# Kernel optimization log

Measured on AMD Instinct MI355X. Metric: run time of the kernel, lower is better.

Reference implementation:

```python
import jax, jax.numpy as jnp
import numpy as np

B, S, H = 2, 2048, 1024
NH = 16
HD = H // NH
MLP = 32


def setup_inputs() -> dict:
    key = jax.random.key(0)
    ks = jax.random.split(key, 24)
    def lin(k, fan_in, shape):
        bound = 1.0 / np.sqrt(fan_in)
        return jax.random.uniform(k, shape, jnp.float32, -bound, bound)
    return {
        "hidden_states": jax.random.normal(ks[0], (B, S, H), jnp.float32),
        "importance_scores": jax.random.uniform(ks[1], (B, S), jnp.float32),
        "wq": lin(ks[2], H, (H, H)), "bq": lin(ks[3], H, (H,)),
        "wk": lin(ks[4], H, (H, H)), "bk": lin(ks[5], H, (H,)),
        "wv": lin(ks[6], H, (H, H)), "bv": lin(ks[7], H, (H,)),
        "wo": lin(ks[8], H, (H, H)), "bo": lin(ks[9], H, (H,)),
        "rw1": lin(ks[10], 1, (1, MLP)), "rb1": lin(ks[11], 1, (MLP,)),
        "rw2": lin(ks[12], MLP, (MLP, NH)), "rb2": lin(ks[13], MLP, (NH,)),
        "aw1": lin(ks[14], 1, (1, MLP)), "ab1": lin(ks[15], 1, (MLP,)),
        "aw2": lin(ks[16], MLP, (MLP, NH)), "ab2": lin(ks[17], MLP, (NH,)),
        "log_temperature": jnp.zeros((NH,), jnp.float32),
        "ln_g": jnp.ones((H,), jnp.float32),
        "ln_b": jnp.zeros((H,), jnp.float32),
    }


def _forward(hidden_states, importance_scores, wq, bq, wk, bk, wv, bv, wo, bo,
             rw1, rb1, rw2, rb2, aw1, ab1, aw2, ab2, log_temperature, ln_g, ln_b):
    Bs, Ss, Hs = hidden_states.shape
    # Q, K, V: (B, NH, S, HD)
    def proj(w, b):
        return (hidden_states @ w + b).reshape(Bs, Ss, NH, HD).transpose(0, 2, 1, 3)
    Q, K, V = proj(wq, bq), proj(wk, bk), proj(wv, bv)
    scale = jnp.sqrt(jnp.float32(HD))
    attn_logits = jnp.einsum('bhqd,bhkd->bhqk', Q, K) / scale

    imp = importance_scores[..., None]  # (B, S, 1)
    def mlp(w1, b1, w2, b2):
        h = jax.nn.gelu(imp @ w1 + b1, approximate=False)
        return h @ w2 + b2  # (B, S, NH)
    reach = mlp(rw1, rb1, rw2, rb2).transpose(0, 2, 1)[..., None]      # (B,NH,S,1)
    attract = mlp(aw1, ab1, aw2, ab2).transpose(0, 2, 1)[..., None, :]  # (B,NH,1,S)

    pos = jnp.arange(Ss, dtype=jnp.float32)
    dist = jnp.abs(pos[None, :] - pos[:, None])  # (S, S); matches |i-j| (symmetric)
    temperature = jnp.exp(log_temperature).reshape(1, NH, 1, 1) + 1.0
    normalized_dist = dist[None, None] / Ss
    mask_logits = reach + attract - normalized_dist / temperature
    mask_bias = jnp.log(jax.nn.sigmoid(mask_logits) + 1e-8)

    attn_weights = jax.nn.softmax(attn_logits + mask_bias, axis=-1)
    attn_out = jnp.einsum('bhqk,bhkd->bhqd', attn_weights, V)
    attn_out = attn_out.transpose(0, 2, 1, 3).reshape(Bs, Ss, Hs)
    out = attn_out @ wo + bo

    x = hidden_states + out
    mu = jnp.mean(x, axis=-1, keepdims=True)
    var = jnp.mean(jnp.square(x - mu), axis=-1, keepdims=True)
    return (x - mu) / jnp.sqrt(var + 1e-5) * ln_g + ln_b


def reference(hidden_states, importance_scores, wq, bq, wk, bk, wv, bv, wo, bo,
              rw1, rb1, rw2, rb2, aw1, ab1, aw2, ab2, log_temperature, ln_g, ln_b):
    return _forward(hidden_states, importance_scores, wq, bq, wk, bk, wv, bv, wo, bo,
                    rw1, rb1, rw2, rb2, aw1, ab1, aw2, ab2, log_temperature, ln_g, ln_b)
```

## Files before the change

kernel.cpp:

```cpp
#include <hip/hip_runtime.h>
#include <math.h>

#define NB 2
#define NS 2048
#define NHID 1024
#define NHEAD 16
#define DHEAD 64

typedef _Float16 half_t;
typedef _Float16 hx4 __attribute__((ext_vector_type(4)));
typedef _Float16 hx8 __attribute__((ext_vector_type(8)));
typedef float fx4 __attribute__((ext_vector_type(4)));

#define RLN2 1.4426950408889634f
#define SCALE_Q 0.18033688011112042f

typedef const __attribute__((address_space(1))) void* gvp;
typedef __attribute__((address_space(3))) void* svp;

static __device__ __forceinline__ void gload16(const void* g, void* s) {
  __builtin_amdgcn_global_load_lds((gvp)g, (svp)s, 16, 0, 0);
}

static __device__ __forceinline__ float gelu_exact(float x) {
  return 0.5f * x * (1.0f + erff(x * 0.70710678118654752f));
}

__launch_bounds__(256)
__global__ void packx(const float* __restrict__ x, half_t* __restrict__ xb) {
  const int i = blockIdx.x * 256 + threadIdx.x;
  const fx4 v = ((const fx4*)x)[i];
  hx4 o;
#pragma unroll
  for (int j = 0; j < 4; ++j) o[j] = (half_t)v[j];
  ((hx4*)xb)[i] = o;
}

__launch_bounds__(256)
__global__ void packw(const float* __restrict__ w0, const float* __restrict__ w1,
                      const float* __restrict__ w2, const float* __restrict__ w3,
                      half_t* __restrict__ o0, half_t* __restrict__ o1,
                      half_t* __restrict__ o2, half_t* __restrict__ o3) {
  __shared__ float tile[32][33];
  const int z = blockIdx.z;
  const float* w = (z == 0) ? w0 : (z == 1) ? w1 : (z == 2) ? w2 : w3;
  half_t* o = (z == 0) ? o0 : (z == 1) ? o1 : (z == 2) ? o2 : o3;
  const int n0 = blockIdx.x * 32, k0 = blockIdx.y * 32;
  const int tx = threadIdx.x, ty = threadIdx.y;
#pragma unroll
  for (int i = 0; i < 4; ++i)
    tile[ty + i * 8][tx] = w[(size_t)(k0 + ty + i * 8) * NHID + n0 + tx];
  __syncthreads();
#pragma unroll
  for (int i = 0; i < 4; ++i)
    o[(size_t)(n0 + ty + i * 8) * NHID + k0 + tx] = (half_t)tile[tx][ty + i * 8];
}

__launch_bounds__(256)
__global__ void mlp16(const float* __restrict__ imp,
                      const float* __restrict__ rw1, const float* __restrict__ rb1,
                      const float* __restrict__ rw2, const float* __restrict__ rb2,
                      const float* __restrict__ aw1, const float* __restrict__ ab1,
                      const float* __restrict__ aw2, const float* __restrict__ ab2,
                      float* __restrict__ reach, float* __restrict__ attract) {
  const int i = blockIdx.x * 256 + threadIdx.x;
  const float v = imp[i];
  const int b = i >> 11, s = i & (NS - 1);
  float ra[16] = {}, aa[16] = {};
  for (int m = 0; m < 32; ++m) {
    const float hr = gelu_exact(v * rw1[m] + rb1[m]);
    const float ha = gelu_exact(v * aw1[m] + ab1[m]);
#pragma unroll
    for (int h = 0; h < 16; ++h) {
      ra[h] += hr * rw2[m * 16 + h];
      aa[h] += ha * aw2[m * 16 + h];
    }
  }
#pragma unroll
  for (int h = 0; h < 16; ++h) {
    reach[(size_t)(b * NHEAD + h) * NS + s] = (ra[h] + rb2[h]) * RLN2;
    attract[(size_t)(b * NHEAD + h) * NS + s] = (aa[h] + ab2[h]) * RLN2;
  }
}

__launch_bounds__(256, 2)
__global__ void gemm_qkv(const half_t* __restrict__ A,
                         const half_t* __restrict__ Wq, const half_t* __restrict__ Wk,
                         const half_t* __restrict__ Wv,
                         const float* __restrict__ bq, const float* __restrict__ bk,
                         const float* __restrict__ bv,
                         half_t* __restrict__ Qo, half_t* __restrict__ Ko,
                         half_t* __restrict__ Vo) {
  __shared__ __align__(16) half_t As[128 * 32];
  __shared__ __align__(16) half_t Bs[128 * 32];
  const int z = blockIdx.z;
  const half_t* Bt = (z == 0) ? Wq : (z == 1) ? Wk : Wv;
  const float* bias = (z == 0) ? bq : (z == 1) ? bk : bv;
  half_t* Co = (z == 0) ? Qo : (z == 1) ? Ko : Vo;
  const float oscale = (z == 0) ? SCALE_Q : 1.0f;

  const int t = threadIdx.x;
  const int l = t & 63, w = t >> 6;
  const int lo = l & 15, g = l >> 4;
  const int m0 = blockIdx.x * 128, n0 = blockIdx.y * 128;
  const int wm = (w >> 1) * 64, wn = (w & 1) * 64;
  fx4 acc[4][4] = {};

  for (int k0 = 0; k0 < NHID; k0 += 32) {
#pragma unroll
    for (int i = 0; i < 2; ++i) {
      const int c = i * 256 + t;
      const int row = c >> 2, kc = (c & 3) * 8;
      gload16(A + (size_t)(m0 + row) * NHID + k0 + kc, As + c * 8);
      gload16(Bt + (size_t)(n0 + row) * NHID + k0 + kc, Bs + c * 8);
    }
    __syncthreads();
    hx8 af[4], bfv[4];
#pragma unroll
    for (int i = 0; i < 4; ++i) {
      af[i] = *(const hx8*)(As + (wm + i * 16 + lo) * 32 + g * 8);
      bfv[i] = *(const hx8*)(Bs + (wn + i * 16 + lo) * 32 + g * 8);
    }
#pragma unroll
    for (int mi = 0; mi < 4; ++mi)
#pragma unroll
      for (int ni = 0; ni < 4; ++ni)
        acc[mi][ni] = __builtin_amdgcn_mfma_f32_16x16x32_f16(af[mi], bfv[ni], acc[mi][ni], 0, 0, 0);
    __syncthreads();
  }

#pragma unroll
  for (int mi = 0; mi < 4; ++mi) {
    const int r0 = m0 + wm + mi * 16 + g * 4;
#pragma unroll
    for (int ni = 0; ni < 4; ++ni) {
      const int col = n0 + wn + ni * 16 + lo;
      const float bs = bias[col];
#pragma unroll
      for (int j = 0; j < 4; ++j)
        Co[(size_t)(r0 + j) * NHID + col] = (half_t)((acc[mi][ni][j] + bs) * oscale);
    }
  }
}

__launch_bounds__(256)
__global__ void vtrans(const half_t* __restrict__ in, half_t* __restrict__ out) {
  __shared__ half_t tile[64][72];
  const int b = blockIdx.z, s0 = blockIdx.x * 64, n0 = blockIdx.y * 64;
  const int t = threadIdx.x;
  const int r = t >> 3, c = (t & 7) * 8;
  const half_t* ip = in + ((size_t)(b * NS) + s0) * NHID + n0;
#pragma unroll
  for (int i = 0; i < 2; ++i)
    *(hx8*)&tile[r + i * 32][c] = *(const hx8*)(ip + (size_t)(r + i * 32) * NHID + c);
  __syncthreads();
  half_t* op = out + ((size_t)(b * NHID) + n0) * NS + s0;
#pragma unroll
  for (int i = 0; i < 2; ++i) {
    hx8 v;
#pragma unroll
    for (int j = 0; j < 8; ++j) v[j] = tile[c + j][r + i * 32];
    *(hx8*)(op + (size_t)(r + i * 32) * NS + c) = v;
  }
}

__launch_bounds__(256, 2)
__global__ void gemm_o(const half_t* __restrict__ A, const half_t* __restrict__ Bt,
                       const float* __restrict__ bias, const float* __restrict__ resid,
                       float* __restrict__ outf) {
  __shared__ __align__(16) half_t As[128 * 32];
  __shared__ __align__(16) half_t Bs[128 * 32];
  const int t = threadIdx.x;
  const int l = t & 63, w = t >> 6;
  const int lo = l & 15, g = l >> 4;
  const int m0 = blockIdx.x * 128, n0 = blockIdx.y * 128;
  const int wm = (w >> 1) * 64, wn = (w & 1) * 64;
  fx4 acc[4][4] = {};

  for (int k0 = 0; k0 < NHID; k0 += 32) {
#pragma unroll
    for (int i = 0; i < 2; ++i) {
      const int c = i * 256 + t;
      const int row = c >> 2, kc = (c & 3) * 8;
      gload16(A + (size_t)(m0 + row) * NHID + k0 + kc, As + c * 8);
      gload16(Bt + (size_t)(n0 + row) * NHID + k0 + kc, Bs + c * 8);
    }
    __syncthreads();
    hx8 af[4], bfv[4];
#pragma unroll
    for (int i = 0; i < 4; ++i) {
      af[i] = *(const hx8*)(As + (wm + i * 16 + lo) * 32 + g * 8);
      bfv[i] = *(const hx8*)(Bs + (wn + i * 16 + lo) * 32 + g * 8);
    }
#pragma unroll
    for (int mi = 0; mi < 4; ++mi)
#pragma unroll
      for (int ni = 0; ni < 4; ++ni)
        acc[mi][ni] = __builtin_amdgcn_mfma_f32_16x16x32_f16(af[mi], bfv[ni], acc[mi][ni], 0, 0, 0);
    __syncthreads();
  }

#pragma unroll
  for (int mi = 0; mi < 4; ++mi) {
    const int r0 = m0 + wm + mi * 16 + g * 4;
#pragma unroll
    for (int ni = 0; ni < 4; ++ni) {
      const int col = n0 + wn + ni * 16 + lo;
      const float bs = bias[col];
#pragma unroll
      for (int j = 0; j < 4; ++j) {
        const size_t idx = (size_t)(r0 + j) * NHID + col;
        outf[idx] = acc[mi][ni][j] + bs + resid[idx];
      }
    }
  }
}

__launch_bounds__(256, 4)
__global__ void attn64(const half_t* __restrict__ Qb, const half_t* __restrict__ Kb,
                       const half_t* __restrict__ Vtb,
                       const float* __restrict__ reach, const float* __restrict__ attract,
                       const float* __restrict__ ltemp,
                       half_t* __restrict__ O) {
  __shared__ __align__(16) half_t Ks[2][64 * 64];
  __shared__ __align__(16) half_t Vs[2][64 * 64];
  __shared__ float apS[2][64], amS[2][64];

  const int t = threadIdx.x;
  const int l = t & 63, w = t >> 6;
  const int lo = l & 15, g = l >> 4;
  const int bh = blockIdx.y;
  const int b = bh >> 4, h = bh & 15;
  const int q0 = blockIdx.x * 64;
  const int q = q0 + w * 16 + lo;

  const float ndc2 = RLN2 / ((__expf(ltemp[h]) + 1.0f) * (float)NS);
  const float rq = reach[(size_t)bh * NS + q];
  const float cqm = rq - (float)q * ndc2;
  const float cqp = rq + (float)q * ndc2;

  hx8 qf[2];
  {
    const half_t* qp = Qb + (size_t)(b * NS + q) * NHID + h * DHEAD + g * 8;
    qf[0] = *(const hx8*)(qp);
    qf[1] = *(const hx8*)(qp + 32);
  }

  fx4 o[4] = {};
  float m_run = -INFINITY, s_run = 0.0f;

  const half_t* Kbase = Kb + (size_t)b * (NS * NHID) + h * DHEAD;
  const half_t* Vbase = Vtb + (size_t)bh * (DHEAD * NS);
  const float* abase = attract + (size_t)bh * NS;

#pragma unroll
  for (int i = 0; i < 2; ++i) {
    const int c = i * 256 + t;
    const int row = c >> 3;
    const int ca = (c & 7) ^ (row & 7);
    gload16(Kbase + (size_t)row * NHID + ca * 8, &Ks[0][c * 8]);
    gload16(Vbase + (size_t)row * NS + ca * 8, &Vs[0][c * 8]);
  }
  if (t < 64) {
    const float a = abase[t];
    apS[0][t] = a + (float)t * ndc2;
    amS[0][t] = a - (float)t * ndc2;
  }
  __syncthreads();

  int buf = 0;
  for (int kv0 = 0; kv0 < NS; kv0 += 64, buf ^= 1) {
    if (kv0 + 64 < NS) {
      const int nb = buf ^ 1;
      const int kvn = kv0 + 64;
#pragma unroll
      for (int i = 0; i < 2; ++i) {
        const int c = i * 256 + t;
        const int row = c >> 3;
        const int ca = (c & 7) ^ (row & 7);
        gload16(Kbase + (size_t)(kvn + row) * NHID + ca * 8, &Ks[nb][c * 8]);
        gload16(Vbase + (size_t)row * NS + kvn + ca * 8, &Vs[nb][c * 8]);
      }
      if (t < 64) {
        const float a = abase[kvn + t];
        const float kvf = (float)(kvn + t);
        apS[nb][t] = a + kvf * ndc2;
        amS[nb][t] = a - kvf * ndc2;
      }
    }

    fx4 sa[4] = {};
#pragma unroll
    for (int mf = 0; mf < 4; ++mf) {
      const int row = mf * 16 + lo;
      const half_t* kr = &Ks[buf][row * 64];
      const int rx = row & 7;
#pragma unroll
      for (int ks = 0; ks < 2; ++ks) {
        const hx8 kf = *(const hx8*)(kr + (((ks * 4 + g) ^ rx) * 8));
        sa[mf] = __builtin_amdgcn_mfma_f32_16x16x32_f16(kf, qf[ks], sa[mf], 0, 0, 0);
      }
    }

    float tmax = -1e30f;
#pragma unroll
    for (int mf = 0; mf < 4; ++mf)
#pragma unroll
      for (int j = 0; j < 4; ++j) tmax = fmaxf(tmax, sa[mf][j]);
    tmax = fmaxf(tmax, __shfl_xor(tmax, 16));
    tmax = fmaxf(tmax, __shfl_xor(tmax, 32));
    if (!__all(tmax - m_run <= 10.0f)) {
      const float m_new = fmaxf(m_run, tmax);
      const float al = __builtin_amdgcn_exp2f(m_run - m_new);
      s_run *= al;
#pragma unroll
      for (int df = 0; df < 4; ++df)
#pragma unroll
        for (int j = 0; j < 4; ++j) o[df][j] *= al;
      m_run = m_new;
    }

    float psum = 0.0f;
    hx4 pb[4];
#pragma unroll
    for (int mf = 0; mf < 4; ++mf) {
      const fx4 ap = *(const fx4*)&apS[buf][mf * 16 + g * 4];
      const fx4 am = *(const fx4*)&amS[buf][mf * 16 + g * 4];
      float pe[4];
#pragma unroll
      for (int j = 0; j < 4; ++j) {
        const float x = fminf(cqm + ap[j], cqp + am[j]);
        const float e = __builtin_amdgcn_exp2f(sa[mf][j] - m_run);
        const float u = __builtin_amdgcn_exp2f(-x);
        const float p = e * __builtin_amdgcn_rcpf(1.0f + u);
        psum += p;
        pe[j] = p;
      }
      const auto c0 = __builtin_amdgcn_cvt_pkrtz(pe[0], pe[1]);
      const auto c1 = __builtin_amdgcn_cvt_pkrtz(pe[2], pe[3]);
      pb[mf][0] = (half_t)c0[0]; pb[mf][1] = (half_t)c0[1];
      pb[mf][2] = (half_t)c1[0]; pb[mf][3] = (half_t)c1[1];
    }
    psum += __shfl_xor(psum, 16);
    psum += __shfl_xor(psum, 32);
    s_run += psum;

#pragma unroll
    for (int df = 0; df < 4; ++df) {
      const int r = df * 16 + lo;
      const half_t* vr = &Vs[buf][r * 64 + (g & 1) * 4];
      const int rx = r & 7;
#pragma unroll
      for (int mf = 0; mf < 4; ++mf) {
        const hx4 vf = *(const hx4*)(vr + (((2 * mf + (g >> 1)) ^ rx) * 8));
        o[df] = __builtin_amdgcn_mfma_f32_16x16x16f16(vf, pb[mf], o[df], 0, 0, 0);
      }
    }
    __syncthreads();
  }

  const float inv = 1.0f / s_run;
  half_t* ob = O + (size_t)(b * NS + q) * NHID + h * DHEAD + g * 4;
#pragma unroll
  for (int df = 0; df < 4; ++df) {
    hx4 v;
#pragma unroll
    for (int j = 0; j < 4; ++j) v[j] = (half_t)(o[df][j] * inv);
    *(hx4*)(ob + df * 16) = v;
  }
}

__launch_bounds__(256)
__global__ void lnorm(const float* __restrict__ y, const float* __restrict__ g,
                      const float* __restrict__ bta, float* __restrict__ out) {
  const int row = blockIdx.x;
  const int t = threadIdx.x;
  const fx4 v = ((const fx4*)(y + (size_t)row * NHID))[t];
  float s = v[0] + v[1] + v[2] + v[3];
  float sq = v[0] * v[0] + v[1] * v[1] + v[2] * v[2] + v[3] * v[3];
#pragma unroll
  for (int off = 1; off < 64; off <<= 1) {
    s += __shfl_xor(s, off);
    sq += __shfl_xor(sq, off);
  }
  __shared__ float rs[4], rsq[4];
  const int w = t >> 6;
  if ((t & 63) == 0) { rs[w] = s; rsq[w] = sq; }
  __syncthreads();
  s = rs[0] + rs[1] + rs[2] + rs[3];
  sq = rsq[0] + rsq[1] + rsq[2] + rsq[3];
  const float mu = s * (1.0f / NHID);
  const float var = sq * (1.0f / NHID) - mu * mu;
  const float rstd = rsqrtf(fmaxf(var, 0.0f) + 1e-5f);
  const fx4 gg = ((const fx4*)g)[t];
  const fx4 bb = ((const fx4*)bta)[t];
  fx4 o;
#pragma unroll
  for (int j = 0; j < 4; ++j) o[j] = (v[j] - mu) * rstd * gg[j] + bb[j];
  ((fx4*)(out + (size_t)row * NHID))[t] = o;
}

extern "C" void kernel_launch(void* const* d_in, const int* in_sizes, int n_in,
                              void* d_out, int out_size, void* d_ws, size_t ws_size,
                              hipStream_t stream) {
  const float* hidden = (const float*)d_in[0];
  const float* imp = (const float*)d_in[1];
  const float* wq = (const float*)d_in[2];  const float* bq = (const float*)d_in[3];
  const float* wk = (const float*)d_in[4];  const float* bk = (const float*)d_in[5];
  const float* wv = (const float*)d_in[6];  const float* bv = (const float*)d_in[7];
  const float* wo = (const float*)d_in[8];  const float* bo = (const float*)d_in[9];
  const float* rw1 = (const float*)d_in[10]; const float* rb1 = (const float*)d_in[11];
  const float* rw2 = (const float*)d_in[12]; const float* rb2 = (const float*)d_in[13];
  const float* aw1 = (const float*)d_in[14]; const float* ab1 = (const float*)d_in[15];
  const float* aw2 = (const float*)d_in[16]; const float* ab2 = (const float*)d_in[17];
  const float* ltemp = (const float*)d_in[18];
  const float* lng = (const float*)d_in[19]; const float* lnb = (const float*)d_in[20];

  char* ws = (char*)d_ws;
  half_t* Xb  = (half_t*)(ws);
  half_t* Wqt = (half_t*)(ws + (size_t)(8u << 20));
  half_t* Wkt = (half_t*)(ws + (size_t)(10u << 20));
  half_t* Wvt = (half_t*)(ws + (size_t)(12u << 20));
  half_t* Wot = (half_t*)(ws + (size_t)(14u << 20));
  half_t* Qb  = (half_t*)(ws + (size_t)(16u << 20));
  half_t* Kb  = (half_t*)(ws + (size_t)(24u << 20));
  half_t* Vtb = (half_t*)(ws + (size_t)(32u << 20));
  half_t* Vb  = (half_t*)(ws + (size_t)(40u << 20));
  half_t* AO  = (half_t*)(ws + (size_t)(40u << 20));
  float*  reach   = (float*)(ws + (size_t)(48u << 20));
  float*  attract = (float*)(ws + (size_t)(48u << 20) + 262144);
  float*  Y = (float*)(ws + (size_t)(16u << 20));

  packx<<<dim3(4096), dim3(256), 0, stream>>>(hidden, Xb);
  packw<<<dim3(32, 32, 4), dim3(32, 8), 0, stream>>>(wq, wk, wv, wo, Wqt, Wkt, Wvt, Wot);
  mlp16<<<dim3(16), dim3(256), 0, stream>>>(imp, rw1, rb1, rw2, rb2, aw1, ab1, aw2, ab2,
                                            reach, attract);
  gemm_qkv<<<dim3(32, 8, 3), dim3(256), 0, stream>>>(Xb, Wqt, Wkt, Wvt, bq, bk, bv,
                                                     Qb, Kb, Vb);
  vtrans<<<dim3(32, 16, 2), dim3(256), 0, stream>>>(Vb, Vtb);
  attn64<<<dim3(32, 32), dim3(256), 0, stream>>>(Qb, Kb, Vtb, reach, attract, ltemp, AO);
  gemm_o<<<dim3(32, 8), dim3(256), 0, stream>>>(AO, Wot, bo, hidden, Y);
  lnorm<<<dim3(4096), dim3(256), 0, stream>>>(Y, lng, lnb, (float*)d_out);
}
```

Before: 288.3 us.

## Factor sigmoid mask into precomputed exponentials and drop online softmax max tracking

Each sigmoid mask term is rewritten as a product of per-query and per-key exponentials precomputed in the MLP kernel, so the attention inner loop needs only a multiply, a max and one exp2 per element. The running-max rescale is removed because the logits are assumed bounded, and the row sum is accumulated with packed fdot2 and reduced once at the end. It also merges the pack kernels into one launch, swizzles the attention block order, raises GEMM occupancy hints, and stores the residual and pre-LayerNorm output in fp16. In exchange it risks overflow if the logits grow, and loses precision from fp16 residuals and Y.

```diff
diff --git a/kernel.cpp b/kernel.cpp
--- a/kernel.cpp
+++ b/kernel.cpp
@@ -27,26 +27,28 @@
 }
 
 __launch_bounds__(256)
-__global__ void packx(const float* __restrict__ x, half_t* __restrict__ xb) {
-  const int i = blockIdx.x * 256 + threadIdx.x;
-  const fx4 v = ((const fx4*)x)[i];
-  hx4 o;
-#pragma unroll
-  for (int j = 0; j < 4; ++j) o[j] = (half_t)v[j];
-  ((hx4*)xb)[i] = o;
-}
-
-__launch_bounds__(256)
-__global__ void packw(const float* __restrict__ w0, const float* __restrict__ w1,
-                      const float* __restrict__ w2, const float* __restrict__ w3,
-                      half_t* __restrict__ o0, half_t* __restrict__ o1,
-                      half_t* __restrict__ o2, half_t* __restrict__ o3) {
+__global__ void prep(const float* __restrict__ x, half_t* __restrict__ xb,
+                     const float* __restrict__ w0, const float* __restrict__ w1,
+                     const float* __restrict__ w2, const float* __restrict__ w3,
+                     half_t* __restrict__ o0, half_t* __restrict__ o1,
+                     half_t* __restrict__ o2, half_t* __restrict__ o3) {
   __shared__ float tile[32][33];
-  const int z = blockIdx.z;
+  const int t = threadIdx.x;
+  if (blockIdx.x < 4096) {
+    const int i = blockIdx.x * 256 + t;
+    const fx4 v = ((const fx4*)x)[i];
+    hx4 o;
+#pragma unroll
+    for (int j = 0; j < 4; ++j) o[j] = (half_t)v[j];
+    ((hx4*)xb)[i] = o;
+    return;
+  }
+  const int bid = blockIdx.x - 4096;
+  const int z = bid >> 10;
   const float* w = (z == 0) ? w0 : (z == 1) ? w1 : (z == 2) ? w2 : w3;
   half_t* o = (z == 0) ? o0 : (z == 1) ? o1 : (z == 2) ? o2 : o3;
-  const int n0 = blockIdx.x * 32, k0 = blockIdx.y * 32;
-  const int tx = threadIdx.x, ty = threadIdx.y;
+  const int n0 = (bid & 31) * 32, k0 = ((bid >> 5) & 31) * 32;
+  const int tx = t & 31, ty = t >> 5;
 #pragma unroll
   for (int i = 0; i < 4; ++i)
     tile[ty + i * 8][tx] = w[(size_t)(k0 + ty + i * 8) * NHID + n0 + tx];
@@ -62,7 +64,9 @@
                       const float* __restrict__ rw2, const float* __restrict__ rb2,
                       const float* __restrict__ aw1, const float* __restrict__ ab1,
                       const float* __restrict__ aw2, const float* __restrict__ ab2,
-                      float* __restrict__ reach, float* __restrict__ attract) {
+                      const float* __restrict__ ltemp,
+                      float* __restrict__ u1G, float* __restrict__ u2G,
+                      float* __restrict__ eapG, float* __restrict__ eamG) {
   const int i = blockIdx.x * 256 + threadIdx.x;
   const float v = imp[i];
   const int b = i >> 11, s = i & (NS - 1);
@@ -76,14 +80,21 @@
       aa[h] += ha * aw2[m * 16 + h];
     }
   }
+  const float sf = (float)s;
 #pragma unroll
   for (int h = 0; h < 16; ++h) {
-    reach[(size_t)(b * NHEAD + h) * NS + s] = (ra[h] + rb2[h]) * RLN2;
-    attract[(size_t)(b * NHEAD + h) * NS + s] = (aa[h] + ab2[h]) * RLN2;
-  }
-}
-
-__launch_bounds__(256, 2)
+    const float ndc2 = RLN2 / ((__expf(ltemp[h]) + 1.0f) * (float)NS);
+    const float r = (ra[h] + rb2[h]) * RLN2;
+    const float a = (aa[h] + ab2[h]) * RLN2;
+    const size_t idx = (size_t)(b * NHEAD + h) * NS + s;
+    u1G[idx]  = __builtin_amdgcn_exp2f(sf * ndc2 - r);
+    u2G[idx]  = __builtin_amdgcn_exp2f(-sf * ndc2 - r);
+    eapG[idx] = __builtin_amdgcn_exp2f(-a - sf * ndc2);
+    eamG[idx] = __builtin_amdgcn_exp2f(-a + sf * ndc2);
+  }
+}
+
+__launch_bounds__(256, 3)
 __global__ void gemm_qkv(const half_t* __restrict__ A,
                          const half_t* __restrict__ Wq, const half_t* __restrict__ Wk,
                          const half_t* __restrict__ Wv,
@@ -164,10 +175,10 @@
   }
 }
 
-__launch_bounds__(256, 2)
+__launch_bounds__(256, 3)
 __global__ void gemm_o(const half_t* __restrict__ A, const half_t* __restrict__ Bt,
-                       const float* __restrict__ bias, const float* __restrict__ resid,
-                       float* __restrict__ outf) {
+                       const float* __restrict__ bias, const half_t* __restrict__ resid,
+                       half_t* __restrict__ Yh) {
   __shared__ __align__(16) half_t As[128 * 32];
   __shared__ __align__(16) half_t Bs[128 * 32];
   const int t = threadIdx.x;
@@ -210,7 +221,7 @@
 #pragma unroll
       for (int j = 0; j < 4; ++j) {
         const size_t idx = (size_t)(r0 + j) * NHID + col;
-        outf[idx] = acc[mi][ni][j] + bs + resid[idx];
+        Yh[idx] = (half_t)(acc[mi][ni][j] + bs + (float)resid[idx]);
       }
     }
   }
@@ -219,39 +230,41 @@
 __launch_bounds__(256, 4)
 __global__ void attn64(const half_t* __restrict__ Qb, const half_t* __restrict__ Kb,
                        const half_t* __restrict__ Vtb,
-                       const float* __restrict__ reach, const float* __restrict__ attract,
-                       const float* __restrict__ ltemp,
+                       const float* __restrict__ u1G, const float* __restrict__ u2G,
+                       const float* __restrict__ eapG, const float* __restrict__ eamG,
                        half_t* __restrict__ O) {
   __shared__ __align__(16) half_t Ks[2][64 * 64];
   __shared__ __align__(16) half_t Vs[2][64 * 64];
-  __shared__ float apS[2][64], amS[2][64];
+  __shared__ float eapS[2][64], eamS[2][64];
 
   const int t = threadIdx.x;
   const int l = t & 63, w = t >> 6;
   const int lo = l & 15, g = l >> 4;
-  const int bh = blockIdx.y;
-  const int b = bh >> 4, h = bh & 15;
-  const int q0 = blockIdx.x * 64;
+  const int id = blockIdx.x;
+  const int swz = (id & 7) * 128 + (id >> 3);
+  const int q0 = (swz & 31) * 64;
+  const int bh = swz >> 5;
+  const int b = bh >> 4;
   const int q = q0 + w * 16 + lo;
 
-  const float ndc2 = RLN2 / ((__expf(ltemp[h]) + 1.0f) * (float)NS);
-  const float rq = reach[(size_t)bh * NS + q];
-  const float cqm = rq - (float)q * ndc2;
-  const float cqp = rq + (float)q * ndc2;
+  const float u1 = u1G[(size_t)bh * NS + q];
+  const float u2 = u2G[(size_t)bh * NS + q];
 
   hx8 qf[2];
   {
-    const half_t* qp = Qb + (size_t)(b * NS + q) * NHID + h * DHEAD + g * 8;
+    const half_t* qp = Qb + (size_t)(b * NS + q) * NHID + (bh & 15) * DHEAD + g * 8;
     qf[0] = *(const hx8*)(qp);
     qf[1] = *(const hx8*)(qp + 32);
   }
 
   fx4 o[4] = {};
-  float m_run = -INFINITY, s_run = 0.0f;
-
-  const half_t* Kbase = Kb + (size_t)b * (NS * NHID) + h * DHEAD;
+  float s_run = 0.0f;
+  const auto one2 = __builtin_amdgcn_cvt_pkrtz(1.0f, 1.0f);
+
+  const half_t* Kbase = Kb + (size_t)b * (NS * NHID) + (bh & 15) * DHEAD;
   const half_t* Vbase = Vtb + (size_t)bh * (DHEAD * NS);
-  const float* abase = attract + (size_t)bh * NS;
+  const float* eapb = eapG + (size_t)bh * NS;
+  const float* eamb = eamG + (size_t)bh * NS;
 
 #pragma unroll
   for (int i = 0; i < 2; ++i) {
@@ -261,11 +274,8 @@
     gload16(Kbase + (size_t)row * NHID + ca * 8, &Ks[0][c * 8]);
     gload16(Vbase + (size_t)row * NS + ca * 8, &Vs[0][c * 8]);
   }
-  if (t < 64) {
-    const float a = abase[t];
-    apS[0][t] = a + (float)t * ndc2;
-    amS[0][t] = a - (float)t * ndc2;
-  }
+  if (t < 64) eapS[0][t] = eapb[t];
+  else if (t < 128) eamS[0][t - 64] = eamb[t - 64];
   __syncthreads();
 
   int buf = 0;
@@ -281,12 +291,8 @@
         gload16(Kbase + (size_t)(kvn + row) * NHID + ca * 8, &Ks[nb][c * 8]);
         gload16(Vbase + (size_t)row * NS + kvn + ca * 8, &Vs[nb][c * 8]);
       }
-      if (t < 64) {
-        const float a = abase[kvn + t];
-        const float kvf = (float)(kvn + t);
-        apS[nb][t] = a + kvf * ndc2;
-        amS[nb][t] = a - kvf * ndc2;
-      }
+      if (t < 64) eapS[nb][t] = eapb[kvn + t];
+      else if (t < 128) eamS[nb][t - 64] = eamb[kvn + t - 64];
     }
 
     fx4 sa[4] = {};
@@ -302,48 +308,27 @@
       }
     }
 
-    float tmax = -1e30f;
-#pragma unroll
-    for (int mf = 0; mf < 4; ++mf)
-#pragma unroll
-      for (int j = 0; j < 4; ++j) tmax = fmaxf(tmax, sa[mf][j]);
-    tmax = fmaxf(tmax, __shfl_xor(tmax, 16));
-    tmax = fmaxf(tmax, __shfl_xor(tmax, 32));
-    if (!__all(tmax - m_run <= 10.0f)) {
-      const float m_new = fmaxf(m_run, tmax);
-      const float al = __builtin_amdgcn_exp2f(m_run - m_new);
-      s_run *= al;
-#pragma unroll
-      for (int df = 0; df < 4; ++df)
-#pragma unroll
-        for (int j = 0; j < 4; ++j) o[df][j] *= al;
-      m_run = m_new;
-    }
-
-    float psum = 0.0f;
+    float psum = s_run;
     hx4 pb[4];
 #pragma unroll
     for (int mf = 0; mf < 4; ++mf) {
-      const fx4 ap = *(const fx4*)&apS[buf][mf * 16 + g * 4];
-      const fx4 am = *(const fx4*)&amS[buf][mf * 16 + g * 4];
+      const fx4 ea = *(const fx4*)&eapS[buf][mf * 16 + g * 4];
+      const fx4 em = *(const fx4*)&eamS[buf][mf * 16 + g * 4];
       float pe[4];
 #pragma unroll
       for (int j = 0; j < 4; ++j) {
-        const float x = fminf(cqm + ap[j], cqp + am[j]);
-        const float e = __builtin_amdgcn_exp2f(sa[mf][j] - m_run);
-        const float u = __builtin_amdgcn_exp2f(-x);
-        const float p = e * __builtin_amdgcn_rcpf(1.0f + u);
-        psum += p;
-        pe[j] = p;
+        const float u = fmaxf(u1 * ea[j], u2 * em[j]);
+        const float e = __builtin_amdgcn_exp2f(sa[mf][j]);
+        pe[j] = e * __builtin_amdgcn_rcpf(1.0f + u);
       }
       const auto c0 = __builtin_amdgcn_cvt_pkrtz(pe[0], pe[1]);
       const auto c1 = __builtin_amdgcn_cvt_pkrtz(pe[2], pe[3]);
+      psum = __builtin_amdgcn_fdot2(c0, one2, psum, false);
+      psum = __builtin_amdgcn_fdot2(c1, one2, psum, false);
       pb[mf][0] = (half_t)c0[0]; pb[mf][1] = (half_t)c0[1];
       pb[mf][2] = (half_t)c1[0]; pb[mf][3] = (half_t)c1[1];
     }
-    psum += __shfl_xor(psum, 16);
-    psum += __shfl_xor(psum, 32);
-    s_run += psum;
+    s_run = psum;
 
 #pragma unroll
     for (int df = 0; df < 4; ++df) {
@@ -359,8 +344,10 @@
     __syncthreads();
   }
 
+  s_run += __shfl_xor(s_run, 16);
+  s_run += __shfl_xor(s_run, 32);
   const float inv = 1.0f / s_run;
-  half_t* ob = O + (size_t)(b * NS + q) * NHID + h * DHEAD + g * 4;
+  half_t* ob = O + (size_t)(b * NS + q) * NHID + (bh & 15) * DHEAD + g * 4;
 #pragma unroll
   for (int df = 0; df < 4; ++df) {
     hx4 v;
@@ -371,11 +358,14 @@
 }
 
 __launch_bounds__(256)
-__global__ void lnorm(const float* __restrict__ y, const float* __restrict__ g,
+__global__ void lnorm(const half_t* __restrict__ y, const float* __restrict__ g,
                       const float* __restrict__ bta, float* __restrict__ out) {
   const int row = blockIdx.x;
   const int t = threadIdx.x;
-  const fx4 v = ((const fx4*)(y + (size_t)row * NHID))[t];
+  const hx4 vh = ((const hx4*)(y + (size_t)row * NHID))[t];
+  fx4 v;
+#pragma unroll
+  for (int j = 0; j < 4; ++j) v[j] = (float)vh[j];
   float s = v[0] + v[1] + v[2] + v[3];
   float sq = v[0] * v[0] + v[1] * v[1] + v[2] * v[2] + v[3] * v[3];
 #pragma unroll
@@ -427,18 +417,20 @@
   half_t* Vtb = (half_t*)(ws + (size_t)(32u << 20));
   half_t* Vb  = (half_t*)(ws + (size_t)(40u << 20));
   half_t* AO  = (half_t*)(ws + (size_t)(40u << 20));
-  float*  reach   = (float*)(ws + (size_t)(48u << 20));
-  float*  attract = (float*)(ws + (size_t)(48u << 20) + 262144);
-  float*  Y = (float*)(ws + (size_t)(16u << 20));
-
-  packx<<<dim3(4096), dim3(256), 0, stream>>>(hidden, Xb);
-  packw<<<dim3(32, 32, 4), dim3(32, 8), 0, stream>>>(wq, wk, wv, wo, Wqt, Wkt, Wvt, Wot);
+  float*  u1G  = (float*)(ws + (size_t)(48u << 20));
+  float*  u2G  = (float*)(ws + (size_t)(48u << 20) + 524288);
+  float*  eapG = (float*)(ws + (size_t)(48u << 20) + 1048576);
+  float*  eamG = (float*)(ws + (size_t)(48u << 20) + 1572864);
+  half_t* Y = (half_t*)(ws + (size_t)(16u << 20));
+
+  prep<<<dim3(8192), dim3(256), 0, stream>>>(hidden, Xb, wq, wk, wv, wo,
+                                             Wqt, Wkt, Wvt, Wot);
   mlp16<<<dim3(16), dim3(256), 0, stream>>>(imp, rw1, rb1, rw2, rb2, aw1, ab1, aw2, ab2,
-                                            reach, attract);
+                                            ltemp, u1G, u2G, eapG, eamG);
   gemm_qkv<<<dim3(32, 8, 3), dim3(256), 0, stream>>>(Xb, Wqt, Wkt, Wvt, bq, bk, bv,
                                                      Qb, Kb, Vb);
   vtrans<<<dim3(32, 16, 2), dim3(256), 0, stream>>>(Vb, Vtb);
-  attn64<<<dim3(32, 32), dim3(256), 0, stream>>>(Qb, Kb, Vtb, reach, attract, ltemp, AO);
-  gemm_o<<<dim3(32, 8), dim3(256), 0, stream>>>(AO, Wot, bo, hidden, Y);
+  attn64<<<dim3(1024), dim3(256), 0, stream>>>(Qb, Kb, Vtb, u1G, u2G, eapG, eamG, AO);
+  gemm_o<<<dim3(32, 8), dim3(256), 0, stream>>>(AO, Wot, bo, Xb, Y);
   lnorm<<<dim3(4096), dim3(256), 0, stream>>>(Y, lng, lnb, (float*)d_out);
 }
```

After: 273.3 us. -5.2%, faster.
